# Kernel tuning notes

Hardware: AMD Instinct MI355X
Metric: run time of the kernel (lower is better)

Reference implementation:

```python
import jax, jax.numpy as jnp
import numpy as np

N_NODES = 100000
N_EDGES = 1600000
IN_CH = 128
HID = 128


def setup_inputs() -> dict:
    key = jax.random.key(0)
    ks = jax.random.split(key, 8)
    x = jax.random.normal(ks[0], (N_NODES, IN_CH), dtype=jnp.float32)
    edge_index = jax.random.randint(ks[1], (2, N_EDGES), 0, N_NODES, dtype=jnp.int64)
    # GCNConv weights (glorot-ish scale) and biases; readout Linear(HID, 1)
    s1 = 1.0 / np.sqrt(IN_CH)
    s2 = 1.0 / np.sqrt(HID)
    W1 = jax.random.normal(ks[2], (IN_CH, HID), dtype=jnp.float32) * s1
    b1 = jnp.zeros((HID,), dtype=jnp.float32)
    W2 = jax.random.normal(ks[3], (HID, HID), dtype=jnp.float32) * s2
    b2 = jnp.zeros((HID,), dtype=jnp.float32)
    Wout = jax.random.normal(ks[4], (HID, 1), dtype=jnp.float32) * s2
    bout = jnp.zeros((1,), dtype=jnp.float32)
    return {"x": x, "edge_index": edge_index, "W1": W1, "b1": b1,
            "W2": W2, "b2": b2, "Wout": Wout, "bout": bout}


def _gcn_conv(x, W, b, src, dst, norm, n_nodes):
    # x' = D^{-1/2}(A+I)D^{-1/2} (x W) + b   (PyG GCNConv default)
    h = x @ W                                   # [N, out]
    msg = h[src] * norm[:, None]                # gather + edge-wise scale
    agg = jax.ops.segment_sum(msg, dst, num_segments=n_nodes)  # scatter-add
    return agg + b


def reference(x, edge_index, W1, b1, W2, b2, Wout, bout):
    n = x.shape[0]
    loop = jnp.arange(n, dtype=edge_index.dtype)
    src = jnp.concatenate([edge_index[0], loop])  # source nodes j (+ self-loops)
    dst = jnp.concatenate([edge_index[1], loop])  # target nodes i (+ self-loops)
    deg = jax.ops.segment_sum(jnp.ones_like(dst, dtype=x.dtype), dst, num_segments=n)
    dis = jax.lax.rsqrt(deg)  # deg >= 1 due to self-loops
    norm = dis[src] * dis[dst]
    h = jax.nn.relu(_gcn_conv(x, W1, b1, src, dst, norm, n))
    h = jax.nn.relu(_gcn_conv(h, W2, b2, src, dst, norm, n))
    out = h @ Wout + bout                        # [N, 1]
    return jnp.squeeze(out)                      # [N]
```

## Files before the change

### kernel.cpp

```cpp
#include <hip/hip_runtime.h>
#include <hip/hip_fp16.h>
#include <type_traits>

#define NFEAT 128
#define SRC_BITS 17
#define SRC_MASK ((1u << SRC_BITS) - 1u)
#define CHUNK 4096
#define STHREADS 512
#define KG 32

using f16x8 = __attribute__((ext_vector_type(8))) _Float16;
using f32x4 = __attribute__((ext_vector_type(4))) float;

static inline size_t align_up(size_t x, size_t a) { return (x + a - 1) & ~(a - 1); }


__global__ __launch_bounds__(STHREADS) void k_hist(const int* __restrict__ dst,
                                                   int* __restrict__ gh,
                                                   int NBUK, int E) {
  extern __shared__ int h[];
  for (int i = threadIdx.x; i < NBUK; i += STHREADS) h[i] = 0;
  __syncthreads();
  int base = blockIdx.x * CHUNK;
  int end = min(base + CHUNK, E);
  for (int e = base + threadIdx.x; e < end; e += STHREADS)
    atomicAdd(&h[dst[e] >> 6], 1);
  __syncthreads();
  int* out = gh + (size_t)blockIdx.x * NBUK;
  for (int i = threadIdx.x; i < NBUK; i += STHREADS) out[i] = h[i];
}

__global__ __launch_bounds__(256) void k_colscan_part(int* __restrict__ gh,
                                                      int* __restrict__ psum,
                                                      int NBUK, int nblk) {
  int b = blockIdx.y * 256 + threadIdx.x;
  if (b >= NBUK) return;
  int kg = blockIdx.x;
  int k0 = kg * KG, k1 = min(k0 + KG, nblk);
  int run = 0;
  for (int k = k0; k < k1; ++k) {
    int idx = k * NBUK + b;
    int c = gh[idx];
    gh[idx] = run;
    run += c;
  }
  psum[kg * NBUK + b] = run;
}

__global__ __launch_bounds__(256) void k_colscan_fix(int* __restrict__ psum,
                                                     int* __restrict__ tot,
                                                     int NBUK, int NG) {
  int b = blockIdx.x * 256 + threadIdx.x;
  if (b >= NBUK) return;
  int run = 0;
  for (int kg = 0; kg < NG; ++kg) {
    int idx = kg * NBUK + b;
    int c = psum[idx];
    psum[idx] = run;
    run += c;
  }
  tot[b] = run;
}

__global__ __launch_bounds__(256) void k_scanB(const int* __restrict__ tot,
                                               int* __restrict__ rsB,
                                               int NBUK, int E) {
  __shared__ int sd[256];
  int tid = threadIdx.x;
  int chunk = (NBUK + 255) / 256;
  int q0 = tid * chunk, q1 = min(q0 + chunk, NBUK);
  int sum = 0;
  for (int q = q0; q < q1; ++q) sum += tot[q];
  sd[tid] = sum;
  __syncthreads();
  for (int off = 1; off < 256; off <<= 1) {
    int t = (tid >= off) ? sd[tid - off] : 0;
    __syncthreads();
    sd[tid] += t;
    __syncthreads();
  }
  int run = sd[tid] - sum;
  for (int q = q0; q < q1; ++q) {
    int c = tot[q];
    rsB[q] = run;
    run += c;
  }
  if (tid == 255) rsB[NBUK] = E;
}

__global__ __launch_bounds__(STHREADS) void k_scatter(const int* __restrict__ src,
                                                      const int* __restrict__ dst,
                                                      const int* __restrict__ gh,
                                                      const int* __restrict__ psum,
                                                      const int* __restrict__ rsB,
                                                      unsigned* __restrict__ ebuf,
                                                      int NBUK, int E) {
  extern __shared__ int cur[];
  const int* g = gh + (size_t)blockIdx.x * NBUK;
  const int* p = psum + (size_t)(blockIdx.x / KG) * NBUK;
  for (int i = threadIdx.x; i < NBUK; i += STHREADS) cur[i] = rsB[i] + p[i] + g[i];
  __syncthreads();
  int base = blockIdx.x * CHUNK;
  int end = min(base + CHUNK, E);
  for (int e = base + threadIdx.x; e < end; e += STHREADS) {
    int d = dst[e];
    int pos = atomicAdd(&cur[d >> 6], 1);
    ebuf[pos] = (unsigned)src[e] | ((unsigned)(d & 63) << SRC_BITS);
  }
}

__global__ __launch_bounds__(256) void k_fill3(const unsigned* __restrict__ ebuf,
                                               const int* __restrict__ rsB,
                                               int* __restrict__ rs,
                                               float* __restrict__ dis,
                                               int* __restrict__ csrc, int N) {
  __shared__ int hist[64];
  __shared__ int curs[64];
  int b = blockIdx.x;
  int node0 = b << 6;
  int nn = min(64, N - node0);
  int base = rsB[b], end = rsB[b + 1];
  int tid = threadIdx.x;
  if (tid < 64) hist[tid] = 0;
  __syncthreads();
  for (int e = base + tid; e < end; e += 256)
    atomicAdd(&hist[ebuf[e] >> SRC_BITS], 1);
  __syncthreads();
  if (tid == 0) {
    int run = base;
    #pragma unroll
    for (int i = 0; i < 64; ++i) {
      int c = hist[i];
      curs[i] = run;
      hist[i] = run;
      run += c;
    }
  }
  __syncthreads();
  if (tid < nn) {
    int start = hist[tid];
    int nxt = (tid == nn - 1) ? end : hist[tid + 1];
    rs[node0 + tid] = start;
    dis[node0 + tid] = rsqrtf((float)(nxt - start) + 1.0f);
  }
  if (tid == 0) rs[node0 + nn] = end;
  for (int e = base + tid; e < end; e += 256) {
    unsigned u = ebuf[e];
    int pos = atomicAdd(&curs[u >> SRC_BITS], 1);
    csrc[pos] = (int)(u & SRC_MASK);
  }
}


__global__ __launch_bounds__(256) void k_wt2(const float* __restrict__ W1,
                                             const float* __restrict__ W2,
                                             __half* __restrict__ W1t,
                                             __half* __restrict__ W2t) {
  const float* W = blockIdx.x ? W2 : W1;
  __half* Wt = blockIdx.x ? W2t : W1t;
  int t = threadIdx.x;
  for (int i = 0; i < 64; ++i) {
    int e = i * 256 + t;
    int r = e >> 7, c = e & 127;
    Wt[c * 128 + r] = __float2half(W[e]);
  }
}


#define XS_LD 136

template <typename T>
__global__ __launch_bounds__(256) void k_gemm(const T* __restrict__ X,
                                              const __half* __restrict__ Wt,
                                              const float* __restrict__ dis,
                                              __half* __restrict__ P, int N) {
  __shared__ __half Xs[64 * XS_LD];
  __shared__ __half Ws[128 * XS_LD];
  const int tid = threadIdx.x;
  const int wave = tid >> 6, lane = tid & 63;
  const int l15 = lane & 15, g = lane >> 4;
  const int rowBase = blockIdx.x * 64;

  #pragma unroll
  for (int it = 0; it < 8; ++it) {
    int q = it * 256 + tid;
    int r = q >> 4, c = (q & 15) * 8;
    *(int4*)&Ws[r * XS_LD + c] = *(const int4*)(Wt + r * 128 + c);
  }
  if constexpr (std::is_same_v<T, float>) {
    #pragma unroll
    for (int it = 0; it < 8; ++it) {
      int q = it * 256 + tid;
      int r = q >> 5, c = (q & 31) * 4;
      int gr = rowBase + r;
      float4 v = make_float4(0.f, 0.f, 0.f, 0.f);
      if (gr < N) v = *(const float4*)(X + (size_t)gr * NFEAT + c);
      __half2 pk[2];
      pk[0] = __floats2half2_rn(v.x, v.y);
      pk[1] = __floats2half2_rn(v.z, v.w);
      *(uint2*)&Xs[r * XS_LD + c] = *(uint2*)pk;
    }
  } else {
    #pragma unroll
    for (int it = 0; it < 4; ++it) {
      int q = it * 256 + tid;
      int r = q >> 4, c = (q & 15) * 8;
      int gr = rowBase + r;
      int4 v = make_int4(0, 0, 0, 0);
      if (gr < N) v = *(const int4*)(X + (size_t)gr * NFEAT + c);
      *(int4*)&Xs[r * XS_LD + c] = v;
    }
  }
  __syncthreads();

  f32x4 acc[4][2];
  #pragma unroll
  for (int rt = 0; rt < 4; ++rt) {
    acc[rt][0] = (f32x4)(0.f);
    acc[rt][1] = (f32x4)(0.f);
  }
  const int koff = g * 8;
  const int c0 = (wave * 2) * 16 + l15;
  const int c1 = (wave * 2 + 1) * 16 + l15;

  #pragma unroll
  for (int ks = 0; ks < 4; ++ks) {
    int kb = ks * 32 + koff;
    f16x8 b0 = *(const f16x8*)&Ws[c0 * XS_LD + kb];
    f16x8 b1 = *(const f16x8*)&Ws[c1 * XS_LD + kb];
    #pragma unroll
    for (int rt = 0; rt < 4; ++rt) {
      f16x8 a = *(const f16x8*)&Xs[(rt * 16 + l15) * XS_LD + kb];
      acc[rt][0] = __builtin_amdgcn_mfma_f32_16x16x32_f16(a, b0, acc[rt][0], 0, 0, 0);
      acc[rt][1] = __builtin_amdgcn_mfma_f32_16x16x32_f16(a, b1, acc[rt][1], 0, 0, 0);
    }
  }

  const int colb = wave * 32 + l15;
  #pragma unroll
  for (int rt = 0; rt < 4; ++rt) {
    #pragma unroll
    for (int r = 0; r < 4; ++r) {
      int row = rowBase + rt * 16 + g * 4 + r;
      if (row < N) {
        float di = dis[row];
        P[(size_t)row * NFEAT + colb]      = __float2half(di * acc[rt][0][r]);
        P[(size_t)row * NFEAT + colb + 16] = __float2half(di * acc[rt][1][r]);
      }
    }
  }
}


__device__ __forceinline__ float agg_body_h2(const __half* __restrict__ P,
                                             const int* __restrict__ rs,
                                             const int* __restrict__ csrc,
                                             int w, int g, int li, float facc[8]) {
  int e0 = rs[w], e1 = rs[w + 1];
  float di = rsqrtf((float)(e1 - e0) + 1.0f);
  __half2 a0 = __float2half2_rn(0.f), a1 = a0, a2 = a0, a3 = a0;
  __half2 c0 = a0, c1 = a0, c2 = a0, c3 = a0;
  if (g == 0) {
    int4 raw = *(const int4*)(P + (size_t)w * NFEAT + li * 8);
    const __half2* h2 = (const __half2*)&raw;
    a0 = h2[0]; a1 = h2[1]; a2 = h2[2]; a3 = h2[3];
  }
  const int lastc = max(e1 - 1, 0);
  int e = e0 + g;
  int s0 = csrc[min(e, lastc)];
  int s1 = csrc[min(e + 4, lastc)];
  while (e + 4 < e1) {
    int4 r0 = *(const int4*)(P + (size_t)s0 * NFEAT + li * 8);
    int4 r1 = *(const int4*)(P + (size_t)s1 * NFEAT + li * 8);
    e += 8;
    s0 = csrc[min(e, lastc)];
    s1 = csrc[min(e + 4, lastc)];
    const __half2* h0 = (const __half2*)&r0;
    const __half2* h1 = (const __half2*)&r1;
    a0 = __hadd2(a0, h0[0]); a1 = __hadd2(a1, h0[1]);
    a2 = __hadd2(a2, h0[2]); a3 = __hadd2(a3, h0[3]);
    c0 = __hadd2(c0, h1[0]); c1 = __hadd2(c1, h1[1]);
    c2 = __hadd2(c2, h1[2]); c3 = __hadd2(c3, h1[3]);
  }
  if (e < e1) {
    int4 r0 = *(const int4*)(P + (size_t)s0 * NFEAT + li * 8);
    const __half2* h0 = (const __half2*)&r0;
    a0 = __hadd2(a0, h0[0]); a1 = __hadd2(a1, h0[1]);
    a2 = __hadd2(a2, h0[2]); a3 = __hadd2(a3, h0[3]);
  }
  a0 = __hadd2(a0, c0); a1 = __hadd2(a1, c1);
  a2 = __hadd2(a2, c2); a3 = __hadd2(a3, c3);
  float2 f0 = __half22float2(a0), f1 = __half22float2(a1);
  float2 f2 = __half22float2(a2), f3 = __half22float2(a3);
  facc[0] = f0.x; facc[1] = f0.y; facc[2] = f1.x; facc[3] = f1.y;
  facc[4] = f2.x; facc[5] = f2.y; facc[6] = f3.x; facc[7] = f3.y;
  #pragma unroll
  for (int j = 0; j < 8; ++j) {
    float v = facc[j];
    v += __shfl_xor(v, 16, 64);
    v += __shfl_xor(v, 32, 64);
    facc[j] = v;
  }
  return di;
}

__global__ __launch_bounds__(256) void k_agg_relu(const __half* __restrict__ P,
                                                  const int* __restrict__ rs,
                                                  const int* __restrict__ csrc,
                                                  const float* __restrict__ bias,
                                                  __half* __restrict__ Hout, int N) {
  int w = (blockIdx.x * 256 + threadIdx.x) >> 6;
  if (w >= N) return;
  int lane = threadIdx.x & 63;
  int g = lane >> 4, li = lane & 15;
  float acc[8];
  float di = agg_body_h2(P, rs, csrc, w, g, li, acc);
  if (g == 0) {
    float4 b0 = *(const float4*)(bias + li * 8);
    float4 b1 = *(const float4*)(bias + li * 8 + 4);
    __half2 o[4];
    o[0] = __floats2half2_rn(fmaxf(fmaf(di, acc[0], b0.x), 0.f),
                             fmaxf(fmaf(di, acc[1], b0.y), 0.f));
    o[1] = __floats2half2_rn(fmaxf(fmaf(di, acc[2], b0.z), 0.f),
                             fmaxf(fmaf(di, acc[3], b0.w), 0.f));
    o[2] = __floats2half2_rn(fmaxf(fmaf(di, acc[4], b1.x), 0.f),
                             fmaxf(fmaf(di, acc[5], b1.y), 0.f));
    o[3] = __floats2half2_rn(fmaxf(fmaf(di, acc[6], b1.z), 0.f),
                             fmaxf(fmaf(di, acc[7], b1.w), 0.f));
    *(int4*)(Hout + (size_t)w * NFEAT + li * 8) = *(const int4*)o;
  }
}

__global__ __launch_bounds__(256) void k_agg_readout(const __half* __restrict__ P,
                                                     const int* __restrict__ rs,
                                                     const int* __restrict__ csrc,
                                                     const float* __restrict__ bias,
                                                     const float* __restrict__ Wout,
                                                     const float* __restrict__ bout,
                                                     float* __restrict__ out, int N) {
  int w = (blockIdx.x * 256 + threadIdx.x) >> 6;
  if (w >= N) return;
  int lane = threadIdx.x & 63;
  int g = lane >> 4, li = lane & 15;
  float acc[8];
  float di = agg_body_h2(P, rs, csrc, w, g, li, acc);
  float4 b0 = *(const float4*)(bias + li * 8);
  float4 b1 = *(const float4*)(bias + li * 8 + 4);
  float4 w0 = *(const float4*)(Wout + li * 8);
  float4 w1 = *(const float4*)(Wout + li * 8 + 4);
  float p = 0.f;
  p = fmaf(fmaxf(fmaf(di, acc[0], b0.x), 0.f), w0.x, p);
  p = fmaf(fmaxf(fmaf(di, acc[1], b0.y), 0.f), w0.y, p);
  p = fmaf(fmaxf(fmaf(di, acc[2], b0.z), 0.f), w0.z, p);
  p = fmaf(fmaxf(fmaf(di, acc[3], b0.w), 0.f), w0.w, p);
  p = fmaf(fmaxf(fmaf(di, acc[4], b1.x), 0.f), w1.x, p);
  p = fmaf(fmaxf(fmaf(di, acc[5], b1.y), 0.f), w1.y, p);
  p = fmaf(fmaxf(fmaf(di, acc[6], b1.z), 0.f), w1.z, p);
  p = fmaf(fmaxf(fmaf(di, acc[7], b1.w), 0.f), w1.w, p);
  p += __shfl_down(p, 8, 64);
  p += __shfl_down(p, 4, 64);
  p += __shfl_down(p, 2, 64);
  p += __shfl_down(p, 1, 64);
  if (lane == 0) out[w] = p + bout[0];
}


extern "C" void kernel_launch(void* const* d_in, const int* in_sizes, int n_in,
                              void* d_out, int out_size, void* d_ws, size_t ws_size,
                              hipStream_t stream) {
  const float* x    = (const float*)d_in[0];
  const int*   ei   = (const int*)d_in[1];
  const float* W1   = (const float*)d_in[2];
  const float* b1   = (const float*)d_in[3];
  const float* W2   = (const float*)d_in[4];
  const float* b2   = (const float*)d_in[5];
  const float* Wout = (const float*)d_in[6];
  const float* bout = (const float*)d_in[7];
  float* out = (float*)d_out;

  const int N = in_sizes[0] / NFEAT;
  const int E = in_sizes[1] / 2;
  const int* src = ei;
  const int* dst = ei + E;
  const int NBUK = (N + 63) >> 6;
  const int nblk = (E + CHUNK - 1) / CHUNK;
  const int NG = (nblk + KG - 1) / KG;

  char* ws = (char*)d_ws;
  size_t off = 0;
  auto alloc = [&](size_t bytes) -> char* {
    char* p = ws + off;
    off = align_up(off + bytes, 256);
    return p;
  };
  int*      gh    = (int*)alloc((size_t)nblk * NBUK * 4);
  int*      psum  = (int*)alloc((size_t)NG * NBUK * 4);
  int*      tot   = (int*)alloc((size_t)NBUK * 4);
  int*      rsB   = (int*)alloc((size_t)(NBUK + 1) * 4);
  int*      rs    = (int*)alloc((size_t)(N + 1) * 4);
  float*    dis   = (float*)alloc((size_t)N * 4);
  unsigned* ebuf  = (unsigned*)alloc((size_t)E * 4);
  int*      csrc  = (int*)alloc((size_t)E * 4);
  __half*   W1t   = (__half*)alloc((size_t)NFEAT * NFEAT * 2);
  __half*   W2t   = (__half*)alloc((size_t)NFEAT * NFEAT * 2);
  __half*   P     = (__half*)alloc((size_t)N * NFEAT * 2);
  __half*   H     = (__half*)alloc((size_t)N * NFEAT * 2);
  (void)ws_size; (void)n_in; (void)out_size;

  const size_t ldsBuk = (size_t)NBUK * 4;
  const int bukBlks = (NBUK + 255) / 256;

  k_wt2<<<2, 256, 0, stream>>>(W1, W2, W1t, W2t);
  k_hist<<<nblk, STHREADS, ldsBuk, stream>>>(dst, gh, NBUK, E);
  k_colscan_part<<<dim3(NG, bukBlks), 256, 0, stream>>>(gh, psum, NBUK, nblk);
  k_colscan_fix<<<bukBlks, 256, 0, stream>>>(psum, tot, NBUK, NG);
  k_scanB<<<1, 256, 0, stream>>>(tot, rsB, NBUK, E);
  k_scatter<<<nblk, STHREADS, ldsBuk, stream>>>(src, dst, gh, psum, rsB, ebuf, NBUK, E);
  k_fill3<<<NBUK, 256, 0, stream>>>(ebuf, rsB, rs, dis, csrc, N);

  k_gemm<float><<<(N + 63) / 64, 256, 0, stream>>>(x, W1t, dis, P, N);
  k_agg_relu<<<(N + 3) / 4, 256, 0, stream>>>(P, rs, csrc, b1, H, N);
  k_gemm<__half><<<(N + 63) / 64, 256, 0, stream>>>(H, W2t, dis, P, N);
  k_agg_readout<<<(N + 3) / 4, 256, 0, stream>>>(P, rs, csrc, b2, Wout, bout, out, N);
}
```

Measured before the change: 234.5 us.

## Fuse layer-1 aggregation with layer-2 GEMM and parallelize bucket scan

Merges the first aggregation+ReLU kernel with the second GEMM. Each 64-row block aggregates its nodes into LDS and then multiplies by W2 with MFMA, so the hidden activations never go out to global memory and one launch is dropped. A separate buffer is used for the second projection. The serial 64-entry prefix scan in k_fill3 becomes a wave shuffle scan. The cost is less parallelism in the aggregation: each wave handles 16 nodes in sequence inside a 64-row block, which may hurt latency hiding. The output stores are also scalar, uncoalesced half writes.

```diff
diff --git a/kernel.cpp b/kernel.cpp
--- a/kernel.cpp
+++ b/kernel.cpp
@@ -126,15 +126,17 @@
   for (int e = base + tid; e < end; e += 256)
     atomicAdd(&hist[ebuf[e] >> SRC_BITS], 1);
   __syncthreads();
-  if (tid == 0) {
-    int run = base;
+  if (tid < 64) {
+    int c = hist[tid];
+    int x = c;
     #pragma unroll
-    for (int i = 0; i < 64; ++i) {
-      int c = hist[i];
-      curs[i] = run;
-      hist[i] = run;
-      run += c;
-    }
+    for (int off = 1; off < 64; off <<= 1) {
+      int t = __shfl_up(x, off, 64);
+      if (tid >= off) x += t;
+    }
+    int start = base + x - c;
+    curs[tid] = start;
+    hist[tid] = start;
   }
   __syncthreads();
   if (tid < nn) {
@@ -169,11 +171,10 @@
 
 #define XS_LD 136
 
-template <typename T>
-__global__ __launch_bounds__(256) void k_gemm(const T* __restrict__ X,
-                                              const __half* __restrict__ Wt,
-                                              const float* __restrict__ dis,
-                                              __half* __restrict__ P, int N) {
+__global__ __launch_bounds__(256) void k_gemm_f(const float* __restrict__ X,
+                                                const __half* __restrict__ Wt,
+                                                const float* __restrict__ dis,
+                                                __half* __restrict__ P, int N) {
   __shared__ __half Xs[64 * XS_LD];
   __shared__ __half Ws[128 * XS_LD];
   const int tid = threadIdx.x;
@@ -187,29 +188,17 @@
     int r = q >> 4, c = (q & 15) * 8;
     *(int4*)&Ws[r * XS_LD + c] = *(const int4*)(Wt + r * 128 + c);
   }
-  if constexpr (std::is_same_v<T, float>) {
-    #pragma unroll
-    for (int it = 0; it < 8; ++it) {
-      int q = it * 256 + tid;
-      int r = q >> 5, c = (q & 31) * 4;
-      int gr = rowBase + r;
-      float4 v = make_float4(0.f, 0.f, 0.f, 0.f);
-      if (gr < N) v = *(const float4*)(X + (size_t)gr * NFEAT + c);
-      __half2 pk[2];
-      pk[0] = __floats2half2_rn(v.x, v.y);
-      pk[1] = __floats2half2_rn(v.z, v.w);
-      *(uint2*)&Xs[r * XS_LD + c] = *(uint2*)pk;
-    }
-  } else {
-    #pragma unroll
-    for (int it = 0; it < 4; ++it) {
-      int q = it * 256 + tid;
-      int r = q >> 4, c = (q & 15) * 8;
-      int gr = rowBase + r;
-      int4 v = make_int4(0, 0, 0, 0);
-      if (gr < N) v = *(const int4*)(X + (size_t)gr * NFEAT + c);
-      *(int4*)&Xs[r * XS_LD + c] = v;
-    }
+  #pragma unroll
+  for (int it = 0; it < 8; ++it) {
+    int q = it * 256 + tid;
+    int r = q >> 5, c = (q & 31) * 4;
+    int gr = rowBase + r;
+    float4 v = make_float4(0.f, 0.f, 0.f, 0.f);
+    if (gr < N) v = *(const float4*)(X + (size_t)gr * NFEAT + c);
+    __half2 pk[2];
+    pk[0] = __floats2half2_rn(v.x, v.y);
+    pk[1] = __floats2half2_rn(v.z, v.w);
+    *(uint2*)&Xs[r * XS_LD + c] = *(uint2*)pk;
   }
   __syncthreads();
 
@@ -304,32 +293,89 @@
   return di;
 }
 
-__global__ __launch_bounds__(256) void k_agg_relu(const __half* __restrict__ P,
+
+__global__ __launch_bounds__(256) void k_agg_gemm(const __half* __restrict__ P,
                                                   const int* __restrict__ rs,
                                                   const int* __restrict__ csrc,
                                                   const float* __restrict__ bias,
-                                                  __half* __restrict__ Hout, int N) {
-  int w = (blockIdx.x * 256 + threadIdx.x) >> 6;
-  if (w >= N) return;
-  int lane = threadIdx.x & 63;
-  int g = lane >> 4, li = lane & 15;
-  float acc[8];
-  float di = agg_body_h2(P, rs, csrc, w, g, li, acc);
-  if (g == 0) {
-    float4 b0 = *(const float4*)(bias + li * 8);
-    float4 b1 = *(const float4*)(bias + li * 8 + 4);
-    __half2 o[4];
-    o[0] = __floats2half2_rn(fmaxf(fmaf(di, acc[0], b0.x), 0.f),
-                             fmaxf(fmaf(di, acc[1], b0.y), 0.f));
-    o[1] = __floats2half2_rn(fmaxf(fmaf(di, acc[2], b0.z), 0.f),
-                             fmaxf(fmaf(di, acc[3], b0.w), 0.f));
-    o[2] = __floats2half2_rn(fmaxf(fmaf(di, acc[4], b1.x), 0.f),
-                             fmaxf(fmaf(di, acc[5], b1.y), 0.f));
-    o[3] = __floats2half2_rn(fmaxf(fmaf(di, acc[6], b1.z), 0.f),
-                             fmaxf(fmaf(di, acc[7], b1.w), 0.f));
-    *(int4*)(Hout + (size_t)w * NFEAT + li * 8) = *(const int4*)o;
-  }
-}
+                                                  const __half* __restrict__ Wt,
+                                                  const float* __restrict__ dis,
+                                                  __half* __restrict__ Pout, int N) {
+  __shared__ __half Xs[64 * XS_LD];
+  const int tid = threadIdx.x;
+  const int wave = tid >> 6, lane = tid & 63;
+  const int l15 = lane & 15, g = lane >> 4;
+  const int rowBase = blockIdx.x * 64;
+
+  float4 bb0 = *(const float4*)(bias + l15 * 8);
+  float4 bb1 = *(const float4*)(bias + l15 * 8 + 4);
+
+  for (int i = 0; i < 16; ++i) {
+    int lr = wave * 16 + i;
+    int node = rowBase + lr;
+    if (node < N) {
+      float acc[8];
+      float di = agg_body_h2(P, rs, csrc, node, g, l15, acc);
+      if (g == 0) {
+        __half2 o[4];
+        o[0] = __floats2half2_rn(fmaxf(fmaf(di, acc[0], bb0.x), 0.f),
+                                 fmaxf(fmaf(di, acc[1], bb0.y), 0.f));
+        o[1] = __floats2half2_rn(fmaxf(fmaf(di, acc[2], bb0.z), 0.f),
+                                 fmaxf(fmaf(di, acc[3], bb0.w), 0.f));
+        o[2] = __floats2half2_rn(fmaxf(fmaf(di, acc[4], bb1.x), 0.f),
+                                 fmaxf(fmaf(di, acc[5], bb1.y), 0.f));
+        o[3] = __floats2half2_rn(fmaxf(fmaf(di, acc[6], bb1.z), 0.f),
+                                 fmaxf(fmaf(di, acc[7], bb1.w), 0.f));
+        *(int4*)&Xs[lr * XS_LD + l15 * 8] = *(const int4*)o;
+      }
+    } else if (g == 0) {
+      int4 z = make_int4(0, 0, 0, 0);
+      *(int4*)&Xs[lr * XS_LD + l15 * 8] = z;
+    }
+  }
+  __syncthreads();
+
+  const int koff = g * 8;
+  const int c0 = wave * 32 + l15;
+  const int c1 = wave * 32 + 16 + l15;
+  f16x8 bf[4][2];
+  #pragma unroll
+  for (int ks = 0; ks < 4; ++ks) {
+    int kb = ks * 32 + koff;
+    bf[ks][0] = *(const f16x8*)(Wt + c0 * 128 + kb);
+    bf[ks][1] = *(const f16x8*)(Wt + c1 * 128 + kb);
+  }
+  f32x4 acc2[4][2];
+  #pragma unroll
+  for (int rt = 0; rt < 4; ++rt) {
+    acc2[rt][0] = (f32x4)(0.f);
+    acc2[rt][1] = (f32x4)(0.f);
+  }
+  #pragma unroll
+  for (int ks = 0; ks < 4; ++ks) {
+    int kb = ks * 32 + koff;
+    #pragma unroll
+    for (int rt = 0; rt < 4; ++rt) {
+      f16x8 a = *(const f16x8*)&Xs[(rt * 16 + l15) * XS_LD + kb];
+      acc2[rt][0] = __builtin_amdgcn_mfma_f32_16x16x32_f16(a, bf[ks][0], acc2[rt][0], 0, 0, 0);
+      acc2[rt][1] = __builtin_amdgcn_mfma_f32_16x16x32_f16(a, bf[ks][1], acc2[rt][1], 0, 0, 0);
+    }
+  }
+  const int colb = wave * 32 + l15;
+  #pragma unroll
+  for (int rt = 0; rt < 4; ++rt) {
+    #pragma unroll
+    for (int r = 0; r < 4; ++r) {
+      int row = rowBase + rt * 16 + g * 4 + r;
+      if (row < N) {
+        float di = dis[row];
+        Pout[(size_t)row * NFEAT + colb]      = __float2half(di * acc2[rt][0][r]);
+        Pout[(size_t)row * NFEAT + colb + 16] = __float2half(di * acc2[rt][1][r]);
+      }
+    }
+  }
+}
+
 
 __global__ __launch_bounds__(256) void k_agg_readout(const __half* __restrict__ P,
                                                      const int* __restrict__ rs,
@@ -403,8 +449,8 @@
   int*      csrc  = (int*)alloc((size_t)E * 4);
   __half*   W1t   = (__half*)alloc((size_t)NFEAT * NFEAT * 2);
   __half*   W2t   = (__half*)alloc((size_t)NFEAT * NFEAT * 2);
-  __half*   P     = (__half*)alloc((size_t)N * NFEAT * 2);
-  __half*   H     = (__half*)alloc((size_t)N * NFEAT * 2);
+  __half*   P1    = (__half*)alloc((size_t)N * NFEAT * 2);
+  __half*   P2    = (__half*)alloc((size_t)N * NFEAT * 2);
   (void)ws_size; (void)n_in; (void)out_size;
 
   const size_t ldsBuk = (size_t)NBUK * 4;
@@ -418,8 +464,7 @@
   k_scatter<<<nblk, STHREADS, ldsBuk, stream>>>(src, dst, gh, psum, rsB, ebuf, NBUK, E);
   k_fill3<<<NBUK, 256, 0, stream>>>(ebuf, rsB, rs, dis, csrc, N);
 
-  k_gemm<float><<<(N + 63) / 64, 256, 0, stream>>>(x, W1t, dis, P, N);
-  k_agg_relu<<<(N + 3) / 4, 256, 0, stream>>>(P, rs, csrc, b1, H, N);
-  k_gemm<__half><<<(N + 63) / 64, 256, 0, stream>>>(H, W2t, dis, P, N);
-  k_agg_readout<<<(N + 3) / 4, 256, 0, stream>>>(P, rs, csrc, b2, Wout, bout, out, N);
-}
+  k_gemm_f<<<(N + 63) / 64, 256, 0, stream>>>(x, W1t, dis, P1, N);
+  k_agg_gemm<<<(N + 63) / 64, 256, 0, stream>>>(P1, rs, csrc, b1, W2t, dis, P2, N);
+  k_agg_readout<<<(N + 3) / 4, 256, 0, stream>>>(P2, rs, csrc, b2, Wout, bout, out, N);
+}
```

Result: slower. 248.0 us (+5.7%).

## Use 256-node CSR buckets, larger chunks, parallel scan and parallel weight transpose

Applied to the files above, without the earlier changes.

Bucket width for the two-level counting sort grows from 64 to 256 nodes and edges per block double. This shrinks the per-block histogram arrays and the column-scan work. Inside k_fill3 the serial 64-entry prefix sum becomes a parallel 256-wide Hillis-Steele scan. The weight transpose now runs on 32 blocks instead of 2. In exchange there is more LDS atomic contention per bucket and more syncs inside the fill kernel.

```diff
diff --git a/kernel.cpp b/kernel.cpp
--- a/kernel.cpp
+++ b/kernel.cpp
@@ -5,7 +5,8 @@
 #define NFEAT 128
 #define SRC_BITS 17
 #define SRC_MASK ((1u << SRC_BITS) - 1u)
-#define CHUNK 4096
+#define BUKSH 8
+#define CHUNK 8192
 #define STHREADS 512
 #define KG 32
 
@@ -24,7 +25,7 @@
   int base = blockIdx.x * CHUNK;
   int end = min(base + CHUNK, E);
   for (int e = base + threadIdx.x; e < end; e += STHREADS)
-    atomicAdd(&h[dst[e] >> 6], 1);
+    atomicAdd(&h[dst[e] >> BUKSH], 1);
   __syncthreads();
   int* out = gh + (size_t)blockIdx.x * NBUK;
   for (int i = threadIdx.x; i < NBUK; i += STHREADS) out[i] = h[i];
@@ -104,8 +105,8 @@
   int end = min(base + CHUNK, E);
   for (int e = base + threadIdx.x; e < end; e += STHREADS) {
     int d = dst[e];
-    int pos = atomicAdd(&cur[d >> 6], 1);
-    ebuf[pos] = (unsigned)src[e] | ((unsigned)(d & 63) << SRC_BITS);
+    int pos = atomicAdd(&cur[d >> BUKSH], 1);
+    ebuf[pos] = (unsigned)src[e] | ((unsigned)(d & 255) << SRC_BITS);
   }
 }
 
@@ -114,31 +115,33 @@
                                                int* __restrict__ rs,
                                                float* __restrict__ dis,
                                                int* __restrict__ csrc, int N) {
-  __shared__ int hist[64];
-  __shared__ int curs[64];
+  __shared__ int hist[256];
+  __shared__ int curs[256];
+  __shared__ int sd[256];
   int b = blockIdx.x;
-  int node0 = b << 6;
-  int nn = min(64, N - node0);
+  int node0 = b << BUKSH;
+  int nn = min(256, N - node0);
   int base = rsB[b], end = rsB[b + 1];
   int tid = threadIdx.x;
-  if (tid < 64) hist[tid] = 0;
+  hist[tid] = 0;
   __syncthreads();
   for (int e = base + tid; e < end; e += 256)
     atomicAdd(&hist[ebuf[e] >> SRC_BITS], 1);
   __syncthreads();
-  if (tid == 0) {
-    int run = base;
-    #pragma unroll
-    for (int i = 0; i < 64; ++i) {
-      int c = hist[i];
-      curs[i] = run;
-      hist[i] = run;
-      run += c;
-    }
-  }
+  int c = hist[tid];
+  sd[tid] = c;
+  __syncthreads();
+  for (int off = 1; off < 256; off <<= 1) {
+    int t = (tid >= off) ? sd[tid - off] : 0;
+    __syncthreads();
+    sd[tid] += t;
+    __syncthreads();
+  }
+  int start = base + sd[tid] - c;
+  curs[tid] = start;
+  hist[tid] = start;
   __syncthreads();
   if (tid < nn) {
-    int start = hist[tid];
     int nxt = (tid == nn - 1) ? end : hist[tid + 1];
     rs[node0 + tid] = start;
     dis[node0 + tid] = rsqrtf((float)(nxt - start) + 1.0f);
@@ -156,13 +159,15 @@
                                              const float* __restrict__ W2,
                                              __half* __restrict__ W1t,
                                              __half* __restrict__ W2t) {
-  const float* W = blockIdx.x ? W2 : W1;
-  __half* Wt = blockIdx.x ? W2t : W1t;
-  int t = threadIdx.x;
-  for (int i = 0; i < 64; ++i) {
-    int e = i * 256 + t;
-    int r = e >> 7, c = e & 127;
-    Wt[c * 128 + r] = __float2half(W[e]);
+  int m = blockIdx.x >> 4;
+  const float* W = m ? W2 : W1;
+  __half* Wt = m ? W2t : W1t;
+  int o = (blockIdx.x & 15) * 1024 + threadIdx.x * 4;
+  #pragma unroll
+  for (int j = 0; j < 4; ++j) {
+    int oo = o + j;
+    int cdst = oo >> 7, rdst = oo & 127;
+    Wt[oo] = __float2half(W[rdst * 128 + cdst]);
   }
 }
 
@@ -382,7 +387,7 @@
   const int E = in_sizes[1] / 2;
   const int* src = ei;
   const int* dst = ei + E;
-  const int NBUK = (N + 63) >> 6;
+  const int NBUK = (N + 255) >> BUKSH;
   const int nblk = (E + CHUNK - 1) / CHUNK;
   const int NG = (nblk + KG - 1) / KG;
 
@@ -403,14 +408,14 @@
   int*      csrc  = (int*)alloc((size_t)E * 4);
   __half*   W1t   = (__half*)alloc((size_t)NFEAT * NFEAT * 2);
   __half*   W2t   = (__half*)alloc((size_t)NFEAT * NFEAT * 2);
-  __half*   P     = (__half*)alloc((size_t)N * NFEAT * 2);
+  __half*   P1    = (__half*)alloc((size_t)N * NFEAT * 2);
   __half*   H     = (__half*)alloc((size_t)N * NFEAT * 2);
   (void)ws_size; (void)n_in; (void)out_size;
 
   const size_t ldsBuk = (size_t)NBUK * 4;
   const int bukBlks = (NBUK + 255) / 256;
 
-  k_wt2<<<2, 256, 0, stream>>>(W1, W2, W1t, W2t);
+  k_wt2<<<32, 256, 0, stream>>>(W1, W2, W1t, W2t);
   k_hist<<<nblk, STHREADS, ldsBuk, stream>>>(dst, gh, NBUK, E);
   k_colscan_part<<<dim3(NG, bukBlks), 256, 0, stream>>>(gh, psum, NBUK, nblk);
   k_colscan_fix<<<bukBlks, 256, 0, stream>>>(psum, tot, NBUK, NG);
@@ -418,8 +423,8 @@
   k_scatter<<<nblk, STHREADS, ldsBuk, stream>>>(src, dst, gh, psum, rsB, ebuf, NBUK, E);
   k_fill3<<<NBUK, 256, 0, stream>>>(ebuf, rsB, rs, dis, csrc, N);
 
-  k_gemm<float><<<(N + 63) / 64, 256, 0, stream>>>(x, W1t, dis, P, N);
-  k_agg_relu<<<(N + 3) / 4, 256, 0, stream>>>(P, rs, csrc, b1, H, N);
-  k_gemm<__half><<<(N + 63) / 64, 256, 0, stream>>>(H, W2t, dis, P, N);
-  k_agg_readout<<<(N + 3) / 4, 256, 0, stream>>>(P, rs, csrc, b2, Wout, bout, out, N);
-}
+  k_gemm<float><<<(N + 63) / 64, 256, 0, stream>>>(x, W1t, dis, P1, N);
+  k_agg_relu<<<(N + 3) / 4, 256, 0, stream>>>(P1, rs, csrc, b1, H, N);
+  k_gemm<__half><<<(N + 63) / 64, 256, 0, stream>>>(H, W2t, dis, P1, N);
+  k_agg_readout<<<(N + 3) / 4, 256, 0, stream>>>(P1, rs, csrc, b2, Wout, bout, out, N);
+}
```

Result: faster. 221.8 us (-5.4%).
